# Kernel optimization log

Measured on AMD Instinct MI355X. Metric: run time of the kernel, lower is better.

The kernel has to match this reference:

```python
import jax, jax.numpy as jnp
import numpy as np

B, N, C, H, W = 2, 6, 256, 56, 100
Q, E, NH = 900, 256, 8
EPS = 1e-5


def setup_inputs() -> dict:
    key = jax.random.key(0)
    ks = jax.random.split(key, 20)
    s = 0.02
    return {
        "image_features": jax.random.normal(ks[0], (B, N, C, H, W), jnp.float32),
        "lidar2img": jax.random.normal(ks[1], (B, N, 4, 4), jnp.float32),
        "query_table": jax.random.normal(ks[2], (Q, E), jnp.float32) * s,
        "ref_W": jax.random.normal(ks[3], (E, 3), jnp.float32) * s,
        "ref_b": jnp.zeros((3,), jnp.float32),
        "Wq": jax.random.normal(ks[4], (E, E), jnp.float32) * s,
        "bq": jnp.zeros((E,), jnp.float32),
        "Wk": jax.random.normal(ks[5], (E, E), jnp.float32) * s,
        "bk": jnp.zeros((E,), jnp.float32),
        "Wv": jax.random.normal(ks[6], (E, E), jnp.float32) * s,
        "bv": jnp.zeros((E,), jnp.float32),
        "Wo": jax.random.normal(ks[7], (E, E), jnp.float32) * s,
        "bo": jnp.zeros((E,), jnp.float32),
        "ln_g": jnp.ones((E,), jnp.float32),
        "ln_b": jnp.zeros((E,), jnp.float32),
        "box_W": jax.random.normal(ks[8], (E, 10), jnp.float32) * s,
        "box_b": jnp.zeros((10,), jnp.float32),
    }


def _grid_sample_bilinear(feats, grid):
    # feats: (M,C,H,W); grid: (M,P,2) in [-1,1]; align_corners=False, zero padding
    M, Cc, Hh, Ww = feats.shape
    gx, gy = grid[..., 0], grid[..., 1]
    x = ((gx + 1.0) * Ww - 1.0) * 0.5
    y = ((gy + 1.0) * Hh - 1.0) * 0.5
    x0 = jnp.floor(x); y0 = jnp.floor(y)
    wx1 = x - x0; wx0 = 1.0 - wx1
    wy1 = y - y0; wy0 = 1.0 - wy1
    midx = jnp.arange(M)[:, None]

    def gather(xi, yi):
        inb = (xi >= 0) & (xi < Ww) & (yi >= 0) & (yi < Hh)
        xi_c = jnp.clip(xi, 0, Ww - 1).astype(jnp.int32)
        yi_c = jnp.clip(yi, 0, Hh - 1).astype(jnp.int32)
        vals = feats[midx, :, yi_c, xi_c]  # (M,P,C)
        return vals * inb[..., None].astype(feats.dtype)

    out = (gather(x0, y0) * (wx0 * wy0)[..., None]
           + gather(x0 + 1, y0) * (wx1 * wy0)[..., None]
           + gather(x0, y0 + 1) * (wx0 * wy1)[..., None]
           + gather(x0 + 1, y0 + 1) * (wx1 * wy1)[..., None])
    return out  # (M,P,C)


def _layer_norm(x, g, b):
    mu = jnp.mean(x, -1, keepdims=True)
    var = jnp.mean((x - mu) ** 2, -1, keepdims=True)
    return (x - mu) * jax.lax.rsqrt(var + EPS) * g + b


def _forward(image_features, lidar2img, query_table, ref_W, ref_b,
             Wq, bq, Wk, bk, Wv, bv, Wo, bo, ln_g, ln_b, box_W, box_b):
    Bv = image_features.shape[0]
    qe = jnp.broadcast_to(query_table[None], (Bv, Q, E))  # (B,Q,E)

    # Step 1: reference points
    ref3d = jax.nn.sigmoid(qe @ ref_W + ref_b)  # (B,Q,3)

    # Step 2: project 3D -> 2D
    pts_h = jnp.concatenate([ref3d, jnp.ones_like(ref3d[..., :1])], -1)  # (B,Q,4)
    p2h = jnp.einsum('bnij,bqj->bnqi', lidar2img, pts_h)  # (B,N,Q,4)
    z = p2h[..., 2:3]
    pts2d = p2h[..., 0:2] / (jnp.abs(z) + 1e-5)  # (B,N,Q,2)
    zmask = (z > 1e-5)[..., 0]  # (B,N,Q)

    # Step 3: normalize + grid_sample + masked average
    gx = pts2d[..., 0] / (W - 1) * 2.0 - 1.0
    gy = pts2d[..., 1] / (H - 1) * 2.0 - 1.0
    grid = jnp.stack([gx, gy], -1).reshape(Bv * N, Q, 2)
    feats = image_features.reshape(Bv * N, C, H, W)
    samp = _grid_sample_bilinear(feats, grid).reshape(Bv, N, Q, C)
    samp = jnp.transpose(samp, (0, 2, 1, 3))  # (B,Q,N,C)

    valid = (gx > -1) & (gx < 1) & (gy > -1) & (gy < 1)  # (B,N,Q)
    final_mask = (zmask & valid).transpose(0, 2, 1)[..., None]  # (B,Q,N,1)
    samp = samp * final_mask.astype(samp.dtype)
    count = jnp.clip(final_mask.sum(2), 1, None).astype(samp.dtype)  # (B,Q,1)
    tgt = samp.sum(2) / count  # (B,Q,C)

    x = qe + tgt

    # self-attention (torch MultiheadAttention math)
    hd = E // NH
    q = (x @ Wq + bq).reshape(Bv, Q, NH, hd)
    k = (x @ Wk + bk).reshape(Bv, Q, NH, hd)
    v = (x @ Wv + bv).reshape(Bv, Q, NH, hd)
    att = jnp.einsum('bqhd,bkhd->bhqk', q, k) / jnp.sqrt(jnp.float32(hd))
    att = jax.nn.softmax(att, -1)
    o = jnp.einsum('bhqk,bkhd->bqhd', att, v).reshape(Bv, Q, E)
    x = o @ Wo + bo

    out = _layer_norm(x, ln_g, ln_b) @ box_W + box_b  # (B,Q,10)
    return out, ref3d


def reference(image_features, lidar2img, query_table, ref_W, ref_b,
              Wq, bq, Wk, bk, Wv, bv, Wo, bo, ln_g, ln_b, box_W, box_b):
    return _forward(image_features, lidar2img, query_table, ref_W, ref_b,
                    Wq, bq, Wk, bk, Wv, bv, Wo, bo, ln_g, ln_b, box_W, box_b)
```

## Files before the change

kernel.cpp:

```cpp
#include <hip/hip_runtime.h>
#include <math.h>

static constexpr int Bv  = 2;
static constexpr int Ncam= 6;
static constexpr int Cch = 256;
static constexpr int Hh  = 56;
static constexpr int Ww  = 100;
static constexpr int Pn  = Hh * Ww;
static constexpr int Qn  = 900;
static constexpr int En  = 256;
static constexpr int NH  = 8;
static constexpr int HD  = 32;

typedef _Float16 f16x8 __attribute__((ext_vector_type(8)));
typedef _Float16 f16x4 __attribute__((ext_vector_type(4)));
typedef _Float16 f16x2 __attribute__((ext_vector_type(2)));
typedef float    f32x4 __attribute__((ext_vector_type(4)));

__global__ __launch_bounds__(256)
void prelude_kernel(const float* __restrict__ W0, const float* __restrict__ W1,
                    const float* __restrict__ W2, const float* __restrict__ W3,
                    _Float16* __restrict__ wt_out,
                    const float* __restrict__ qt, const float* __restrict__ refW,
                    const float* __restrict__ refb, const float* __restrict__ l2i,
                    float* __restrict__ gridbuf, float* __restrict__ out_ref3d) {
    int bid = blockIdx.x;
    int t = threadIdx.x;
    if (bid < 256) {
        __shared__ float tile[32][33];
        int z = bid >> 6, rem = bid & 63;
        const float* src = (z == 0) ? W0 : (z == 1) ? W1 : (z == 2) ? W2 : W3;
        int k0 = (rem & 7) * 32, n0 = (rem >> 3) * 32;
        int tx = t & 31, ty = t >> 5;
        for (int i = 0; i < 32; i += 8)
            tile[ty + i][tx] = src[(size_t)(k0 + ty + i) * 256 + n0 + tx];
        __syncthreads();
        _Float16* dst = wt_out + (size_t)z * 256 * 256;
        for (int i = 0; i < 32; i += 8)
            dst[(size_t)(n0 + ty + i) * 256 + k0 + tx] = (_Float16)tile[tx][ty + i];
    } else {
        int wave = t >> 6, lane = t & 63;
        int q = (bid - 256) * 4 + wave;
        float s0 = 0.f, s1 = 0.f, s2 = 0.f;
        for (int i = lane; i < En; i += 64) {
            float a = qt[q * En + i];
            s0 += a * refW[i * 3 + 0];
            s1 += a * refW[i * 3 + 1];
            s2 += a * refW[i * 3 + 2];
        }
        for (int off = 32; off > 0; off >>= 1) {
            s0 += __shfl_down(s0, off);
            s1 += __shfl_down(s1, off);
            s2 += __shfl_down(s2, off);
        }
        s0 = __shfl(s0, 0); s1 = __shfl(s1, 0); s2 = __shfl(s2, 0);
        float v0 = 1.f / (1.f + __expf(-(s0 + refb[0])));
        float v1 = 1.f / (1.f + __expf(-(s1 + refb[1])));
        float v2 = 1.f / (1.f + __expf(-(s2 + refb[2])));
        if (lane == 0) {
            out_ref3d[(size_t)q * 3 + 0] = v0;
            out_ref3d[(size_t)q * 3 + 1] = v1;
            out_ref3d[(size_t)q * 3 + 2] = v2;
            out_ref3d[(size_t)(Qn + q) * 3 + 0] = v0;
            out_ref3d[(size_t)(Qn + q) * 3 + 1] = v1;
            out_ref3d[(size_t)(Qn + q) * 3 + 2] = v2;
        }
        if (lane < Bv * Ncam) {
            int b = lane / Ncam, n = lane % Ncam;
            const float* M = l2i + (size_t)(b * Ncam + n) * 16;
            float p0 = M[0] * v0 + M[1] * v1 + M[2]  * v2 + M[3];
            float p1 = M[4] * v0 + M[5] * v1 + M[6]  * v2 + M[7];
            float z  = M[8] * v0 + M[9] * v1 + M[10] * v2 + M[11];
            float denom = fabsf(z) + 1e-5f;
            float px = p0 / denom, py = p1 / denom;
            float gx = px / (float)(Ww - 1) * 2.f - 1.f;
            float gy = py / (float)(Hh - 1) * 2.f - 1.f;
            bool zm = z > 1e-5f;
            bool valid = (gx > -1.f) && (gx < 1.f) && (gy > -1.f) && (gy < 1.f);
            float* g = gridbuf + ((size_t)(b * Ncam + n) * Qn + q) * 3;
            g[0] = gx; g[1] = gy; g[2] = (zm && valid) ? 1.f : 0.f;
        }
    }
}

__global__ __launch_bounds__(256)
void feat_pack_kernel(const float* __restrict__ in, _Float16* __restrict__ outp) {
    __shared__ _Float16 tile[32][132];
    int m = blockIdx.z;
    int p0 = blockIdx.x * 128, c0 = blockIdx.y * 32;
    int t = threadIdx.x;
    {
        int p4 = (t & 31) * 4;
        int cc0 = t >> 5;
        for (int i = 0; i < 4; i++) {
            int cc = cc0 + i * 8;
            int p = p0 + p4;
            if (p < Pn) {
                float4 v = *(const float4*)&in[((size_t)m * Cch + c0 + cc) * Pn + p];
                f16x4 h = {(_Float16)v.x, (_Float16)v.y, (_Float16)v.z, (_Float16)v.w};
                *(f16x4*)&tile[cc][p4] = h;
            }
        }
    }
    __syncthreads();
    {
        int cg = (t & 7) * 4;
        int pr = t >> 3;
        for (int i = 0; i < 4; i++) {
            int pl = pr + i * 32;
            int p = p0 + pl;
            if (p < Pn) {
                f16x4 h;
                h.x = tile[cg + 0][pl];
                h.y = tile[cg + 1][pl];
                h.z = tile[cg + 2][pl];
                h.w = tile[cg + 3][pl];
                *(f16x4*)&outp[((size_t)m * Pn + p) * Cch + c0 + cg] = h;
            }
        }
    }
}

__device__ __forceinline__ void corner_acc2(const _Float16* __restrict__ base,
                                            int xi, int yi, int ch, float w,
                                            float& a0, float& a1) {
    if (xi < 0 || xi >= Ww || yi < 0 || yi >= Hh) return;
    f16x2 v = *(const f16x2*)&base[((size_t)yi * Ww + xi) * Cch + ch];
    a0 += (float)v.x * w;
    a1 += (float)v.y * w;
}

__global__ __launch_bounds__(256)
void sample_kernel(const _Float16* __restrict__ featsT,
                   const float* __restrict__ gridbuf,
                   const float* __restrict__ qt,
                   _Float16* __restrict__ xbuf) {
    int t = threadIdx.x;
    int bq = blockIdx.x * 2 + (t >> 7);
    int b = bq / Qn, q = bq % Qn;
    int ch = (t & 127) * 2;
    float a0 = 0.f, a1 = 0.f, cnt = 0.f;
    for (int n = 0; n < Ncam; n++) {
        const float* g = gridbuf + ((size_t)(b * Ncam + n) * Qn + q) * 3;
        float gx = g[0], gy = g[1], msk = g[2];
        if (msk > 0.5f) {
            cnt += 1.f;
            float x = ((gx + 1.f) * (float)Ww - 1.f) * 0.5f;
            float y = ((gy + 1.f) * (float)Hh - 1.f) * 0.5f;
            float x0f = floorf(x), y0f = floorf(y);
            int x0 = (int)x0f, y0 = (int)y0f;
            float wx1 = x - x0f, wx0 = 1.f - wx1;
            float wy1 = y - y0f, wy0 = 1.f - wy1;
            const _Float16* base = featsT + (size_t)(b * Ncam + n) * Pn * Cch;
            corner_acc2(base, x0,     y0,     ch, wx0 * wy0, a0, a1);
            corner_acc2(base, x0 + 1, y0,     ch, wx1 * wy0, a0, a1);
            corner_acc2(base, x0,     y0 + 1, ch, wx0 * wy1, a0, a1);
            corner_acc2(base, x0 + 1, y0 + 1, ch, wx1 * wy1, a0, a1);
        }
    }
    float inv = 1.f / fmaxf(cnt, 1.f);
    float2 qv = *(const float2*)&qt[(size_t)q * En + ch];
    f16x2 o;
    o.x = (_Float16)(qv.x + a0 * inv);
    o.y = (_Float16)(qv.y + a1 * inv);
    *(f16x2*)&xbuf[(size_t)bq * En + ch] = o;
}

__device__ __forceinline__ void mfma_gemm_body(const _Float16* __restrict__ A,
                                               const _Float16* __restrict__ Wt,
                                               const float* __restrict__ bias,
                                               _Float16* __restrict__ Cf16,
                                               float* __restrict__ Cf32,
                                               int M, int m0, int n0) {
    __shared__ _Float16 Ws[64][264];
    int t = threadIdx.x;
    int wave = t >> 6, lane = t & 63, quad = lane >> 4, col = lane & 15;
    {
        int row = t >> 5;
        int off = (t & 31) * 8;
        for (int i = 0; i < 8; i++)
            *(f16x8*)&Ws[row + i * 8][off] =
                *(const f16x8*)&Wt[(size_t)(n0 + row + i * 8) * 256 + off];
    }
    f16x8 af[8];
    int mrow = m0 + wave * 16 + col;
    if (mrow < M) {
        const _Float16* ap = A + (size_t)mrow * 256 + quad * 8;
        #pragma unroll
        for (int kc = 0; kc < 8; kc++) af[kc] = *(const f16x8*)(ap + kc * 32);
    } else {
        #pragma unroll
        for (int kc = 0; kc < 8; kc++)
            #pragma unroll
            for (int j = 0; j < 8; j++) af[kc][j] = (_Float16)0.f;
    }
    __syncthreads();
    f32x4 acc[4];
    #pragma unroll
    for (int nt = 0; nt < 4; nt++) { acc[nt][0]=0.f; acc[nt][1]=0.f; acc[nt][2]=0.f; acc[nt][3]=0.f; }
    #pragma unroll
    for (int nt = 0; nt < 4; nt++)
        #pragma unroll
        for (int kc = 0; kc < 8; kc++) {
            f16x8 bf = *(const f16x8*)&Ws[nt * 16 + col][kc * 32 + quad * 8];
            acc[nt] = __builtin_amdgcn_mfma_f32_16x16x32_f16(af[kc], bf, acc[nt], 0, 0, 0);
        }
    #pragma unroll
    for (int nt = 0; nt < 4; nt++) {
        int n = n0 + nt * 16 + col;
        float bv = bias[n];
        #pragma unroll
        for (int r = 0; r < 4; r++) {
            int m = m0 + wave * 16 + quad * 4 + r;
            if (m < M) {
                float v = acc[nt][r] + bv;
                if (Cf16) Cf16[(size_t)m * 256 + n] = (_Float16)v;
                else      Cf32[(size_t)m * 256 + n] = v;
            }
        }
    }
}

__global__ __launch_bounds__(256)
void qkv_mfma_kernel(const _Float16* __restrict__ A,
                     const _Float16* __restrict__ Wtall,
                     const float* __restrict__ bq, const float* __restrict__ bk,
                     const float* __restrict__ bv,
                     _Float16* __restrict__ qo, _Float16* __restrict__ ko,
                     _Float16* __restrict__ vo, int M) {
    const _Float16* Wt; const float* bias; _Float16* out;
    if (blockIdx.z == 0)      { Wt = Wtall;                 bias = bq; out = qo; }
    else if (blockIdx.z == 1) { Wt = Wtall + 256 * 256;     bias = bk; out = ko; }
    else                      { Wt = Wtall + 2 * 256 * 256; bias = bv; out = vo; }
    mfma_gemm_body(A, Wt, bias, out, nullptr, M, blockIdx.x * 64, blockIdx.y * 64);
}

__global__ __launch_bounds__(256)
void wo_mfma_kernel(const _Float16* __restrict__ A,
                    const _Float16* __restrict__ Wtall,
                    const float* __restrict__ bo,
                    float* __restrict__ x2, int M) {
    mfma_gemm_body(A, Wtall + 3 * 256 * 256, bo, nullptr, x2, M,
                   blockIdx.x * 64, blockIdx.y * 64);
}

static constexpr int FTQ = 32;
static constexpr int FTK = 64;

__global__ __launch_bounds__(128)
void flash_attn_mfma_kernel(const _Float16* __restrict__ qbuf,
                            const _Float16* __restrict__ kbuf,
                            const _Float16* __restrict__ vbuf,
                            _Float16* __restrict__ obuf) {
    __shared__ _Float16 Ks[FTK][40];
    __shared__ _Float16 Vt[HD][72];
    __shared__ _Float16 Ps[2][16][72];

    int bh = blockIdx.y;
    int b = bh / NH, h = bh % NH;
    int m0 = blockIdx.x * FTQ;
    int t = threadIdx.x;
    int wave = t >> 6, lane = t & 63;
    int quad = lane >> 4, col = lane & 15;

    const float scale = 0.17677669529663687f;

    f16x8 qf;
    {
        int qrow = m0 + wave * 16 + col;
        if (qrow < Qn) {
            qf = *(const f16x8*)(qbuf + ((size_t)b * Qn + qrow) * En + h * HD + quad * 8);
        } else {
            #pragma unroll
            for (int j = 0; j < 8; j++) qf[j] = (_Float16)0.f;
        }
    }

    f32x4 o0 = {0.f, 0.f, 0.f, 0.f};
    f32x4 o1 = {0.f, 0.f, 0.f, 0.f};
    float mrow[4] = {-3e38f, -3e38f, -3e38f, -3e38f};
    float lrow[4] = {0.f, 0.f, 0.f, 0.f};

    int nstage = t >> 1;
    int koff = (t & 1) * 16;

    for (int n0 = 0; n0 < Qn; n0 += FTK) {
        {
            int ng = n0 + nstage;
            f16x8 k0v, k1v, v0v, v1v;
            if (ng < Qn) {
                const _Float16* kp = kbuf + ((size_t)b * Qn + ng) * En + h * HD + koff;
                const _Float16* vp = vbuf + ((size_t)b * Qn + ng) * En + h * HD + koff;
                k0v = *(const f16x8*)kp;  k1v = *(const f16x8*)(kp + 8);
                v0v = *(const f16x8*)vp;  v1v = *(const f16x8*)(vp + 8);
            } else {
                #pragma unroll
                for (int j = 0; j < 8; j++) { k0v[j]=(_Float16)0.f; k1v[j]=(_Float16)0.f;
                                              v0v[j]=(_Float16)0.f; v1v[j]=(_Float16)0.f; }
            }
            *(f16x8*)&Ks[nstage][koff]     = k0v;
            *(f16x8*)&Ks[nstage][koff + 8] = k1v;
            #pragma unroll
            for (int j = 0; j < 8; j++) {
                Vt[koff + j][nstage]     = v0v[j];
                Vt[koff + 8 + j][nstage] = v1v[j];
            }
        }
        __syncthreads();

        f32x4 S[4];
        #pragma unroll
        for (int c = 0; c < 4; c++) {
            f16x8 kf = *(const f16x8*)&Ks[c * 16 + col][quad * 8];
            f32x4 z = {0.f, 0.f, 0.f, 0.f};
            S[c] = __builtin_amdgcn_mfma_f32_16x16x32_f16(qf, kf, z, 0, 0, 0);
            S[c] *= scale;
        }
        if (n0 + FTK > Qn) {
            #pragma unroll
            for (int c = 0; c < 4; c++) {
                if (n0 + c * 16 + col >= Qn) {
                    S[c][0] = -3e38f; S[c][1] = -3e38f; S[c][2] = -3e38f; S[c][3] = -3e38f;
                }
            }
        }

        float p[4][4];
        #pragma unroll
        for (int r = 0; r < 4; r++) {
            float mx = fmaxf(fmaxf(S[0][r], S[1][r]), fmaxf(S[2][r], S[3][r]));
            #pragma unroll
            for (int off = 8; off >= 1; off >>= 1)
                mx = fmaxf(mx, __shfl_xor(mx, off, 64));
            float mnew = fmaxf(mrow[r], mx);
            float alpha = __expf(mrow[r] - mnew);
            mrow[r] = mnew;
            float rs = 0.f;
            #pragma unroll
            for (int c = 0; c < 4; c++) {
                float pv = __expf(S[c][r] - mnew);
                p[c][r] = pv;
                rs += pv;
            }
            #pragma unroll
            for (int off = 8; off >= 1; off >>= 1)
                rs += __shfl_xor(rs, off, 64);
            lrow[r] = lrow[r] * alpha + rs;
            o0[r] *= alpha;
            o1[r] *= alpha;
        }

        #pragma unroll
        for (int c = 0; c < 4; c++)
            #pragma unroll
            for (int r = 0; r < 4; r++)
                Ps[wave][quad * 4 + r][c * 16 + col] = (_Float16)p[c][r];

        #pragma unroll
        for (int kc = 0; kc < 2; kc++) {
            f16x8 pf = *(const f16x8*)&Ps[wave][col][kc * 32 + quad * 8];
            f16x8 v0 = *(const f16x8*)&Vt[col][kc * 32 + quad * 8];
            f16x8 v1 = *(const f16x8*)&Vt[16 + col][kc * 32 + quad * 8];
            o0 = __builtin_amdgcn_mfma_f32_16x16x32_f16(pf, v0, o0, 0, 0, 0);
            o1 = __builtin_amdgcn_mfma_f32_16x16x32_f16(pf, v1, o1, 0, 0, 0);
        }
        __syncthreads();
    }

    #pragma unroll
    for (int r = 0; r < 4; r++) {
        int q = m0 + wave * 16 + quad * 4 + r;
        if (q < Qn) {
            float inv = 1.f / lrow[r];
            _Float16* op = obuf + ((size_t)b * Qn + q) * En + h * HD;
            op[col]      = (_Float16)(o0[r] * inv);
            op[16 + col] = (_Float16)(o1[r] * inv);
        }
    }
}

__global__ void ln_box_kernel(const float* __restrict__ x2,
                              const float* __restrict__ ln_g,
                              const float* __restrict__ ln_b,
                              const float* __restrict__ boxW,
                              const float* __restrict__ boxb,
                              float* __restrict__ outp) {
    __shared__ float red[256];
    __shared__ float yrow[En];
    __shared__ float pbox[16][10];
    int bq = blockIdx.x;
    int t = threadIdx.x;
    float acc = x2[(size_t)bq * En + t];
    red[t] = acc; __syncthreads();
    for (int s = 128; s > 0; s >>= 1) {
        if (t < s) red[t] += red[t + s];
        __syncthreads();
    }
    float mu = red[0] / (float)En;
    __syncthreads();
    float dx = acc - mu;
    red[t] = dx * dx; __syncthreads();
    for (int s = 128; s > 0; s >>= 1) {
        if (t < s) red[t] += red[t + s];
        __syncthreads();
    }
    float var = red[0] / (float)En;
    float y = dx * rsqrtf(var + 1e-5f) * ln_g[t] + ln_b[t];
    yrow[t] = y;
    __syncthreads();
    if (t < 160) {
        int j = t % 10, ch = t / 10;
        float p = 0.f;
        for (int k = ch * 16; k < ch * 16 + 16; k++)
            p += yrow[k] * boxW[(size_t)k * 10 + j];
        pbox[ch][j] = p;
    }
    __syncthreads();
    if (t < 10) {
        float o = boxb[t];
        for (int ch = 0; ch < 16; ch++) o += pbox[ch][t];
        outp[(size_t)bq * 10 + t] = o;
    }
}

extern "C" void kernel_launch(void* const* d_in, const int* in_sizes, int n_in,
                              void* d_out, int out_size, void* d_ws, size_t ws_size,
                              hipStream_t stream) {
    const float* image_features = (const float*)d_in[0];
    const float* lidar2img      = (const float*)d_in[1];
    const float* query_table    = (const float*)d_in[2];
    const float* ref_W          = (const float*)d_in[3];
    const float* ref_b          = (const float*)d_in[4];
    const float* Wq             = (const float*)d_in[5];
    const float* bq             = (const float*)d_in[6];
    const float* Wk             = (const float*)d_in[7];
    const float* bk             = (const float*)d_in[8];
    const float* Wv             = (const float*)d_in[9];
    const float* bv             = (const float*)d_in[10];
    const float* Wo             = (const float*)d_in[11];
    const float* bo             = (const float*)d_in[12];
    const float* ln_g           = (const float*)d_in[13];
    const float* ln_b           = (const float*)d_in[14];
    const float* box_W          = (const float*)d_in[15];
    const float* box_b          = (const float*)d_in[16];
    float* out = (float*)d_out;

    char* ws = (char*)d_ws;
    size_t off = 0;
    auto alloc = [&](size_t bytes) { char* p = ws + off; off += (bytes + 255) & ~size_t(255); return p; };
    float*     gridbuf = (float*)    alloc((size_t)Bv * Ncam * Qn * 3 * 4);
    _Float16*  featsT  = (_Float16*) alloc((size_t)Bv * Ncam * Pn * Cch * 2);
    _Float16*  xbuf    = (_Float16*) alloc((size_t)Bv * Qn * En * 2);
    _Float16*  qbuf    = (_Float16*) alloc((size_t)Bv * Qn * En * 2);
    _Float16*  kbuf    = (_Float16*) alloc((size_t)Bv * Qn * En * 2);
    _Float16*  vbuf    = (_Float16*) alloc((size_t)Bv * Qn * En * 2);
    _Float16*  obuf    = (_Float16*) alloc((size_t)Bv * Qn * En * 2);
    float*     x2buf   = (float*)    alloc((size_t)Bv * Qn * En * 4);
    _Float16*  Wtall   = (_Float16*) alloc((size_t)4 * 256 * 256 * 2);

    float* out_ref3d = out + (size_t)Bv * Qn * 10;
    int M = Bv * Qn;

    hipLaunchKernelGGL(prelude_kernel, dim3(256 + 225), dim3(256), 0, stream,
                       Wq, Wk, Wv, Wo, Wtall,
                       query_table, ref_W, ref_b, lidar2img, gridbuf, out_ref3d);

    hipLaunchKernelGGL(feat_pack_kernel,
                       dim3((Pn + 127) / 128, Cch / 32, Bv * Ncam), dim3(256),
                       0, stream, image_features, featsT);

    hipLaunchKernelGGL(sample_kernel, dim3(Bv * Qn / 2), dim3(256), 0, stream,
                       featsT, gridbuf, query_table, xbuf);

    hipLaunchKernelGGL(qkv_mfma_kernel, dim3((M + 63) / 64, En / 64, 3), dim3(256),
                       0, stream, xbuf, Wtall, bq, bk, bv, qbuf, kbuf, vbuf, M);

    hipLaunchKernelGGL(flash_attn_mfma_kernel,
                       dim3((Qn + FTQ - 1) / FTQ, Bv * NH), dim3(128), 0, stream,
                       qbuf, kbuf, vbuf, obuf);

    hipLaunchKernelGGL(wo_mfma_kernel, dim3((M + 63) / 64, En / 64), dim3(256),
                       0, stream, obuf, Wtall, bo, x2buf, M);

    hipLaunchKernelGGL(ln_box_kernel, dim3(Bv * Qn), dim3(256), 0, stream,
                       x2buf, ln_g, ln_b, box_W, box_b, out);
}
```

Measured before the change: 185.8 us.

## Sample bilinear corners directly from NCHW fp32 features, drop transpose pack

Removes the kernel that converted the whole image feature tensor (about 34M floats) into an fp16 channel-last copy. Instead, the sampling kernel reads the four bilinear corners directly from the original NCHW fp32 layout, one channel per thread. This avoids a full read and write pass over roughly 140MB of features. In exchange each corner access is now strided by the H*W plane, so loads are uncoalesced scattered 4-byte reads, which costs more per sample.

```diff
diff --git a/kernel.cpp b/kernel.cpp
--- a/kernel.cpp
+++ b/kernel.cpp
@@ -84,62 +84,14 @@
 }
 
 __global__ __launch_bounds__(256)
-void feat_pack_kernel(const float* __restrict__ in, _Float16* __restrict__ outp) {
-    __shared__ _Float16 tile[32][132];
-    int m = blockIdx.z;
-    int p0 = blockIdx.x * 128, c0 = blockIdx.y * 32;
-    int t = threadIdx.x;
-    {
-        int p4 = (t & 31) * 4;
-        int cc0 = t >> 5;
-        for (int i = 0; i < 4; i++) {
-            int cc = cc0 + i * 8;
-            int p = p0 + p4;
-            if (p < Pn) {
-                float4 v = *(const float4*)&in[((size_t)m * Cch + c0 + cc) * Pn + p];
-                f16x4 h = {(_Float16)v.x, (_Float16)v.y, (_Float16)v.z, (_Float16)v.w};
-                *(f16x4*)&tile[cc][p4] = h;
-            }
-        }
-    }
-    __syncthreads();
-    {
-        int cg = (t & 7) * 4;
-        int pr = t >> 3;
-        for (int i = 0; i < 4; i++) {
-            int pl = pr + i * 32;
-            int p = p0 + pl;
-            if (p < Pn) {
-                f16x4 h;
-                h.x = tile[cg + 0][pl];
-                h.y = tile[cg + 1][pl];
-                h.z = tile[cg + 2][pl];
-                h.w = tile[cg + 3][pl];
-                *(f16x4*)&outp[((size_t)m * Pn + p) * Cch + c0 + cg] = h;
-            }
-        }
-    }
-}
-
-__device__ __forceinline__ void corner_acc2(const _Float16* __restrict__ base,
-                                            int xi, int yi, int ch, float w,
-                                            float& a0, float& a1) {
-    if (xi < 0 || xi >= Ww || yi < 0 || yi >= Hh) return;
-    f16x2 v = *(const f16x2*)&base[((size_t)yi * Ww + xi) * Cch + ch];
-    a0 += (float)v.x * w;
-    a1 += (float)v.y * w;
-}
-
-__global__ __launch_bounds__(256)
-void sample_kernel(const _Float16* __restrict__ featsT,
+void sample_kernel(const float* __restrict__ feats,
                    const float* __restrict__ gridbuf,
                    const float* __restrict__ qt,
                    _Float16* __restrict__ xbuf) {
-    int t = threadIdx.x;
-    int bq = blockIdx.x * 2 + (t >> 7);
+    int bq = blockIdx.x;
     int b = bq / Qn, q = bq % Qn;
-    int ch = (t & 127) * 2;
-    float a0 = 0.f, a1 = 0.f, cnt = 0.f;
+    int c = threadIdx.x;
+    float acc = 0.f, cnt = 0.f;
     for (int n = 0; n < Ncam; n++) {
         const float* g = gridbuf + ((size_t)(b * Ncam + n) * Qn + q) * 3;
         float gx = g[0], gy = g[1], msk = g[2];
@@ -151,19 +103,17 @@
             int x0 = (int)x0f, y0 = (int)y0f;
             float wx1 = x - x0f, wx0 = 1.f - wx1;
             float wy1 = y - y0f, wy0 = 1.f - wy1;
-            const _Float16* base = featsT + (size_t)(b * Ncam + n) * Pn * Cch;
-            corner_acc2(base, x0,     y0,     ch, wx0 * wy0, a0, a1);
-            corner_acc2(base, x0 + 1, y0,     ch, wx1 * wy0, a0, a1);
-            corner_acc2(base, x0,     y0 + 1, ch, wx0 * wy1, a0, a1);
-            corner_acc2(base, x0 + 1, y0 + 1, ch, wx1 * wy1, a0, a1);
-        }
-    }
-    float inv = 1.f / fmaxf(cnt, 1.f);
-    float2 qv = *(const float2*)&qt[(size_t)q * En + ch];
-    f16x2 o;
-    o.x = (_Float16)(qv.x + a0 * inv);
-    o.y = (_Float16)(qv.y + a1 * inv);
-    *(f16x2*)&xbuf[(size_t)bq * En + ch] = o;
+            const float* base = feats + ((size_t)(b * Ncam + n) * Cch + c) * Pn;
+            bool xin0 = (x0 >= 0) & (x0 < Ww), xin1 = (x0 + 1 >= 0) & (x0 + 1 < Ww);
+            bool yin0 = (y0 >= 0) & (y0 < Hh), yin1 = (y0 + 1 >= 0) & (y0 + 1 < Hh);
+            if (xin0 & yin0) acc += base[(size_t)y0 * Ww + x0]           * (wx0 * wy0);
+            if (xin1 & yin0) acc += base[(size_t)y0 * Ww + x0 + 1]       * (wx1 * wy0);
+            if (xin0 & yin1) acc += base[(size_t)(y0 + 1) * Ww + x0]     * (wx0 * wy1);
+            if (xin1 & yin1) acc += base[(size_t)(y0 + 1) * Ww + x0 + 1] * (wx1 * wy1);
+        }
+    }
+    float tgt = acc / fmaxf(cnt, 1.f);
+    xbuf[(size_t)bq * En + c] = (_Float16)(qt[(size_t)q * En + c] + tgt);
 }
 
 __device__ __forceinline__ void mfma_gemm_body(const _Float16* __restrict__ A,
@@ -449,7 +399,6 @@
     size_t off = 0;
     auto alloc = [&](size_t bytes) { char* p = ws + off; off += (bytes + 255) & ~size_t(255); return p; };
     float*     gridbuf = (float*)    alloc((size_t)Bv * Ncam * Qn * 3 * 4);
-    _Float16*  featsT  = (_Float16*) alloc((size_t)Bv * Ncam * Pn * Cch * 2);
     _Float16*  xbuf    = (_Float16*) alloc((size_t)Bv * Qn * En * 2);
     _Float16*  qbuf    = (_Float16*) alloc((size_t)Bv * Qn * En * 2);
     _Float16*  kbuf    = (_Float16*) alloc((size_t)Bv * Qn * En * 2);
@@ -465,12 +414,8 @@
                        Wq, Wk, Wv, Wo, Wtall,
                        query_table, ref_W, ref_b, lidar2img, gridbuf, out_ref3d);
 
-    hipLaunchKernelGGL(feat_pack_kernel,
-                       dim3((Pn + 127) / 128, Cch / 32, Bv * Ncam), dim3(256),
-                       0, stream, image_features, featsT);
-
-    hipLaunchKernelGGL(sample_kernel, dim3(Bv * Qn / 2), dim3(256), 0, stream,
-                       featsT, gridbuf, query_table, xbuf);
+    hipLaunchKernelGGL(sample_kernel, dim3(Bv * Qn), dim3(256), 0, stream,
+                       image_features, gridbuf, query_table, xbuf);
 
     hipLaunchKernelGGL(qkv_mfma_kernel, dim3((M + 63) / 64, En / 64, 3), dim3(256),
                        0, stream, xbuf, Wtall, bq, bk, bv, qbuf, kbuf, vbuf, M);
```

Measured after the change: 178.8 us. 3.8% less time.
